# Kernel optimization log

Measured on AMD Instinct MI355X. Metric: run time of the kernel, lower is better.

Reference implementation:

```python
import jax, jax.numpy as jnp
import numpy as np

ANNEALING_SCALE = 0.1
BS, NV, S, D, V = 2, 16, 1024, 768, 50257

def setup_inputs() -> dict:
    key = jax.random.key(0)
    k1, k2, k3, k4, k5 = jax.random.split(key, 5)
    return {
        "input_ids": jax.random.randint(k1, (BS, S), 0, V),
        "content": jax.random.normal(k2, (BS, NV, S, D), dtype=jnp.float32),
        "contextualization": jax.random.normal(k3, (BS, NV, S, S), dtype=jnp.float32) * 0.05,
        "lm_head_weight": jax.random.normal(k4, (V, D), dtype=jnp.float32) * 0.02,
        "content_weights": jax.random.uniform(k5, (V, NV), dtype=jnp.float32),
    }

def reference(input_ids, content, contextualization, lm_head_weight, content_weights):
    bs, nv, s, d = content.shape
    # --- mask_annealing ---
    # Original computes relu(content @ W.T) over full vocab then gathers at input_ids.
    # Equivalent: gather rows of W first, then contract (same math since relu is
    # elementwise and only gathered columns are summed).
    Wg = lm_head_weight[input_ids]                              # (bs, s, d)
    sims = jnp.einsum('bkid,bjd->bkij', content, Wg)            # (bs, 16, s, s)
    sims = jnp.sum(jax.nn.relu(sims), axis=3)                   # (bs, 16, s)
    scores = jax.nn.sigmoid(-ANNEALING_SCALE * sims + 6.0)
    # upweight_nearby modifier
    scores = scores * (1.0 + jnp.arange(s, dtype=content.dtype) / 100.0)[None, None, :]
    scores = jnp.transpose(scores, (0, 2, 1))                   # (bs, s, 16)
    # --- create_content_soft_mask ---
    cw = content_weights[input_ids]                             # (bs, s, 16)
    weights = cw * scores + (1.0 - scores)                      # (bs, s, 16)
    # --- weighted sense combination ---
    content_m = content * jnp.transpose(weights, (0, 2, 1))[..., None]  # (bs,16,s,d)
    hidden = jnp.einsum('bkij,bkjd->bid', contextualization, content_m) # (bs, s, d)
    logits = hidden @ lm_head_weight.T                          # (bs, s, vocab)
    return logits
```

## Files before the change

kernel.cpp:

```cpp
#include <hip/hip_runtime.h>
#include <cstdint>
#include <cstddef>

#define BSZ 2
#define NV 16
#define SEQ 1024
#define DIM 768
#define VOC 50257
#define VOCP 50304

typedef unsigned int u32;
typedef unsigned short u16;
typedef _Float16 half8 __attribute__((ext_vector_type(8)));
typedef float f32x4 __attribute__((ext_vector_type(4)));

__device__ __forceinline__ u16 f2h(float f) {
  return __builtin_bit_cast(unsigned short, (_Float16)f);
}
__device__ __forceinline__ u32 pk2h(float a, float b) {
  return (u32)f2h(a) | ((u32)f2h(b) << 16);
}

__device__ __forceinline__ void gload16(const u16* g, u16* l) {
  __builtin_amdgcn_global_load_lds(
      (const __attribute__((address_space(1))) void*)g,
      (__attribute__((address_space(3))) void*)l, 16, 0, 0);
}

__global__ void k_prep_content(const float* __restrict__ content,
                               u16* __restrict__ cbf, u16* __restrict__ cT) {
  __shared__ u16 tile[32][33];
  const int bk = blockIdx.z;
  const int d0 = blockIdx.x * 32, j0 = blockIdx.y * 32;
  const float* src = content + (size_t)bk * SEQ * DIM;
  u16* dst = cbf + (size_t)bk * SEQ * DIM;
  u16* dstT = cT + (size_t)bk * DIM * SEQ;
  const int c = threadIdx.x;
#pragma unroll
  for (int rr = 0; rr < 4; ++rr) {
    const int r = threadIdx.y * 4 + rr;
    const float v = src[(size_t)(j0 + r) * DIM + d0 + c];
    const u16 bv = f2h(v);
    dst[(size_t)(j0 + r) * DIM + d0 + c] = bv;
    tile[r][c] = bv;
  }
  __syncthreads();
#pragma unroll
  for (int rr = 0; rr < 4; ++rr) {
    const int r = threadIdx.y * 4 + rr;
    dstT[(size_t)(d0 + r) * SEQ + j0 + c] = tile[c][r];
  }
}

__global__ void k_prep_w(const float* __restrict__ W, u16* __restrict__ Wb) {
  const int v = blockIdx.x;
  const int c = threadIdx.x * 4;
  u32 lo, hi;
  if (v < VOC) {
    const float4 f = *(const float4*)(W + (size_t)v * DIM + c);
    lo = pk2h(f.x, f.y); hi = pk2h(f.z, f.w);
  } else {
    lo = 0u; hi = 0u;
  }
  *(uint2*)(Wb + (size_t)v * DIM + c) = make_uint2(lo, hi);
}

__global__ void k_gather(const int* __restrict__ ids, const u16* __restrict__ Wb,
                         u16* __restrict__ Wg) {
  const int b = blockIdx.y, j = blockIdx.x;
  const int row = ids[b * SEQ + j];
  const int c = threadIdx.x * 4;
  *(uint2*)(Wg + ((size_t)b * SEQ + j) * DIM + c) =
      *(const uint2*)(Wb + (size_t)row * DIM + c);
}

__global__ void k_zero(float* __restrict__ p, int n) {
  const int i = blockIdx.x * 256 + threadIdx.x;
  if (i < n) p[i] = 0.f;
}

template <int LDA, int LDB>
__device__ __forceinline__ void gemm_core(const u16* __restrict__ A,
                                          const u16* __restrict__ B, int ksteps,
                                          u16* As, u16* Bs, f32x4 (&acc)[4][4],
                                          int t) {
  const int lane = t & 63, w = t >> 6, wr = w >> 1, wc = w & 1;
  const int rl = lane & 15;
  const int gsw = (((lane >> 4) ^ ((rl >> 1) & 3)) * 8);
  const int srow = 16 * w + (lane >> 2);
  const int sg = (((lane & 3) ^ ((lane >> 3) & 3)) * 8);
  const size_t gaBase = (size_t)srow * LDA + sg;
  const size_t gbBase = (size_t)srow * LDB + sg;
  u16* lA = As + w * 512;
  u16* lB = Bs + w * 512;

#define STAGE_(bb, kt)                                                  \
  {                                                                     \
    const u16* ga_ = A + gaBase + (size_t)(kt) * 32;                    \
    const u16* gb_ = B + gbBase + (size_t)(kt) * 32;                    \
    gload16(ga_, lA + (bb) * 4096);                                     \
    gload16(ga_ + (size_t)64 * LDA, lA + (bb) * 4096 + 2048);           \
    gload16(gb_, lB + (bb) * 4096);                                     \
    gload16(gb_ + (size_t)64 * LDB, lB + (bb) * 4096 + 2048);           \
  }

#define FRAGS_(bb)                                                      \
  half8 af[4], bf[4];                                                   \
  _Pragma("unroll") for (int m = 0; m < 4; ++m)                         \
      af[m] = *(const half8*)(As + (bb) * 4096 +                        \
                              (wr * 64 + m * 16 + rl) * 32 + gsw);      \
  _Pragma("unroll") for (int n = 0; n < 4; ++n)                         \
      bf[n] = *(const half8*)(Bs + (bb) * 4096 +                        \
                              (wc * 64 + n * 16 + rl) * 32 + gsw);      \
  _Pragma("unroll") for (int m = 0; m < 4; ++m)                         \
      _Pragma("unroll") for (int n = 0; n < 4; ++n)                     \
          acc[m][n] = __builtin_amdgcn_mfma_f32_16x16x32_f16(           \
              af[m], bf[n], acc[m][n], 0, 0, 0);

  STAGE_(0, 0);
  __syncthreads();
  int cur = 0;
  for (int kt = 0; kt < ksteps - 1; ++kt) {
    STAGE_(cur ^ 1, kt + 1);
    { FRAGS_(cur); }
    __syncthreads();
    cur ^= 1;
  }
  { FRAGS_(cur); }
#undef STAGE_
#undef FRAGS_
}

template <int LDA, int LDB>
__device__ __forceinline__ void gemm_ring2(const u16* __restrict__ A0,
                                           const u16* __restrict__ A1,
                                           const u16* __restrict__ B, int ksteps,
                                           u16* As0, u16* As1, u16* Bs,
                                           f32x4 (&acc0)[4][4],
                                           f32x4 (&acc1)[4][4], int t) {
  const int lane = t & 63, w = t >> 6, wr = w >> 1, wc = w & 1;
  const int rl = lane & 15;
  const int gsw = (((lane >> 4) ^ ((rl >> 1) & 3)) * 8);
  const int srow = 16 * w + (lane >> 2);
  const int sg = (((lane & 3) ^ ((lane >> 3) & 3)) * 8);
  const size_t gaBase = (size_t)srow * LDA + sg;
  const size_t gbBase = (size_t)srow * LDB + sg;
  const int wof = w * 512;

#define STG3_(ss, kt)                                                   \
  {                                                                     \
    const u16* ga0_ = A0 + gaBase + (size_t)(kt) * 32;                  \
    const u16* ga1_ = A1 + gaBase + (size_t)(kt) * 32;                  \
    const u16* gb_ = B + gbBase + (size_t)(kt) * 32;                    \
    gload16(ga0_, As0 + (ss) * 4096 + wof);                             \
    gload16(ga0_ + (size_t)64 * LDA, As0 + (ss) * 4096 + wof + 2048);   \
    gload16(ga1_, As1 + (ss) * 4096 + wof);                            \
    gload16(ga1_ + (size_t)64 * LDA, As1 + (ss) * 4096 + wof + 2048);   \
    gload16(gb_, Bs + (ss) * 4096 + wof);                              \
    gload16(gb_ + (size_t)64 * LDB, Bs + (ss) * 4096 + wof + 2048);     \
  }

#define FRAGS3_(ss)                                                     \
  half8 af0[4], af1[4], bf[4];                                          \
  _Pragma("unroll") for (int n = 0; n < 4; ++n)                         \
      bf[n] = *(const half8*)(Bs + (ss) * 4096 +                        \
                              (wc * 64 + n * 16 + rl) * 32 + gsw);      \
  _Pragma("unroll") for (int m = 0; m < 4; ++m)                         \
      af0[m] = *(const half8*)(As0 + (ss) * 4096 +                      \
                               (wr * 64 + m * 16 + rl) * 32 + gsw);     \
  _Pragma("unroll") for (int m = 0; m < 4; ++m)                         \
      af1[m] = *(const half8*)(As1 + (ss) * 4096 +                      \
                               (wr * 64 + m * 16 + rl) * 32 + gsw);

#define MFMA32_                                                         \
  __builtin_amdgcn_s_setprio(1);                                        \
  _Pragma("unroll") for (int m = 0; m < 4; ++m)                         \
      _Pragma("unroll") for (int n = 0; n < 4; ++n)                     \
          acc0[m][n] = __builtin_amdgcn_mfma_f32_16x16x32_f16(          \
              af0[m], bf[n], acc0[m][n], 0, 0, 0);                      \
  _Pragma("unroll") for (int m = 0; m < 4; ++m)                         \
      _Pragma("unroll") for (int n = 0; n < 4; ++n)                     \
          acc1[m][n] = __builtin_amdgcn_mfma_f32_16x16x32_f16(          \
              af1[m], bf[n], acc1[m][n], 0, 0, 0);                      \
  __builtin_amdgcn_s_setprio(0);

#define STEPF_(ss, kt)                                                  \
  asm volatile("s_waitcnt vmcnt(6)" ::: "memory");                      \
  __builtin_amdgcn_s_barrier();                                         \
  __builtin_amdgcn_sched_barrier(0);                                    \
  STG3_(((ss) + 2) % 3, (kt) + 2);                                      \
  { FRAGS3_(ss) MFMA32_ }

#define STEPL6_(ss)                                                     \
  asm volatile("s_waitcnt vmcnt(6)" ::: "memory");                      \
  __builtin_amdgcn_s_barrier();                                         \
  __builtin_amdgcn_sched_barrier(0);                                    \
  { FRAGS3_(ss) MFMA32_ }

#define STEPL0_(ss)                                                     \
  asm volatile("s_waitcnt vmcnt(0)" ::: "memory");                      \
  __builtin_amdgcn_s_barrier();                                         \
  __builtin_amdgcn_sched_barrier(0);                                    \
  { FRAGS3_(ss) MFMA32_ }

  STG3_(0, 0);
  STG3_(1, 1);
  const int nTrip = ksteps / 3;
  for (int u = 0; u < nTrip - 1; ++u) {
    const int kt = 3 * u;
    STEPF_(0, kt);
    STEPF_(1, kt + 1);
    STEPF_(2, kt + 2);
  }
  STEPF_(0, ksteps - 3);
  STEPL6_(1);
  STEPL0_(2);
#undef STG3_
#undef FRAGS3_
#undef MFMA32_
#undef STEPF_
#undef STEPL6_
#undef STEPL0_
}

__global__ __launch_bounds__(256, 2) void k_sims(const u16* __restrict__ cbf,
                                                 const u16* __restrict__ Wg,
                                                 float* __restrict__ sims) {
  __shared__ __align__(16) u16 As0[3 * 4096];
  __shared__ __align__(16) u16 As1[3 * 4096];
  __shared__ __align__(16) u16 Bs[3 * 4096];
  const int bk = blockIdx.z, b = bk >> 4;
  const int t = threadIdx.x;
  const int i0 = blockIdx.y * 256;
  const u16* A0 = cbf + (size_t)bk * SEQ * DIM + (size_t)i0 * DIM;
  const u16* A1 = A0 + (size_t)128 * DIM;
  const u16* B = Wg + (size_t)b * SEQ * DIM + (size_t)(blockIdx.x * 128) * DIM;
  f32x4 acc0[4][4] = {}, acc1[4][4] = {};
  gemm_ring2<DIM, DIM>(A0, A1, B, DIM / 32, As0, As1, Bs, acc0, acc1, t);
  const int lane = t & 63, w = t >> 6, wr = w >> 1;
  const int rg = lane >> 4, cl = lane & 15;
#pragma unroll
  for (int m = 0; m < 4; ++m) {
#pragma unroll
    for (int r = 0; r < 4; ++r) {
      float s0 = 0.f, s1 = 0.f;
#pragma unroll
      for (int n = 0; n < 4; ++n) {
        s0 += fmaxf(acc0[m][n][r], 0.f);
        s1 += fmaxf(acc1[m][n][r], 0.f);
      }
      s0 += __shfl_xor(s0, 1); s1 += __shfl_xor(s1, 1);
      s0 += __shfl_xor(s0, 2); s1 += __shfl_xor(s1, 2);
      s0 += __shfl_xor(s0, 4); s1 += __shfl_xor(s1, 4);
      s0 += __shfl_xor(s0, 8); s1 += __shfl_xor(s1, 8);
      if (cl == 0) {
        const int i = i0 + wr * 64 + m * 16 + rg * 4 + r;
        atomicAdd(&sims[(size_t)bk * SEQ + i], s0);
        atomicAdd(&sims[(size_t)bk * SEQ + i + 128], s1);
      }
    }
  }
}

__global__ void k_weights(const float* __restrict__ sims, const int* __restrict__ ids,
                          const float* __restrict__ cw, float* __restrict__ wtsT) {
  const int j = blockIdx.x * 256 + threadIdx.x;
  const int bk = blockIdx.y;
  const int b = bk >> 4, k = bk & 15;
  const float sm = sims[(size_t)bk * SEQ + j];
  float score = 1.f / (1.f + __expf(0.1f * sm - 6.f));
  score *= 1.f + (float)j * 0.01f;
  const int id = ids[b * SEQ + j];
  const float c = cw[(size_t)id * NV + k];
  wtsT[(size_t)bk * SEQ + j] = c * score + (1.f - score);
}

__global__ void k_ctx(const float* __restrict__ ctx, const float* __restrict__ wtsT,
                      u16* __restrict__ ctxw) {
  const size_t i = ((size_t)blockIdx.x * 256 + threadIdx.x) * 4;
  const float4 c = *(const float4*)(ctx + i);
  const size_t bk = i >> 20;
  const int j = (int)(i & (SEQ - 1));
  const float4 wv = *(const float4*)(wtsT + bk * SEQ + j);
  *(uint2*)(ctxw + i) =
      make_uint2(pk2h(c.x * wv.x, c.y * wv.y), pk2h(c.z * wv.z, c.w * wv.w));
}

__global__ __launch_bounds__(256) void k_hidden(const u16* __restrict__ ctxw,
                                                const u16* __restrict__ cT,
                                                float* __restrict__ part) {
  __shared__ __align__(16) u16 As[2 * 128 * 32];
  __shared__ __align__(16) u16 Bs[2 * 128 * 32];
  const int z = blockIdx.z;
  const int b = z >> 2, g = z & 3;
  const int i0 = blockIdx.y * 128, d0 = blockIdx.x * 128;
  const int t = threadIdx.x;
  f32x4 acc[4][4] = {};
  for (int kk = 0; kk < 4; ++kk) {
    const int sense = g * 4 + kk;
    const u16* A = ctxw + ((size_t)(b * NV + sense) * SEQ + i0) * SEQ;
    const u16* B = cT + ((size_t)(b * NV + sense) * DIM + d0) * SEQ;
    gemm_core<SEQ, SEQ>(A, B, SEQ / 32, As, Bs, acc, t);
    __syncthreads();
  }
  const int lane = t & 63, w = t >> 6, wr = w >> 1, wc = w & 1;
  const int rg = lane >> 4, cl = lane & 15;
  float* P = part + ((size_t)(g * BSZ + b) * SEQ + i0) * DIM + d0;
#pragma unroll
  for (int m = 0; m < 4; ++m)
#pragma unroll
    for (int n = 0; n < 4; ++n)
#pragma unroll
      for (int r = 0; r < 4; ++r)
        P[(size_t)(wr * 64 + m * 16 + rg * 4 + r) * DIM + wc * 64 + n * 16 + cl] =
            acc[m][n][r];
}

__global__ void k_reduce(const float* __restrict__ part, u16* __restrict__ hid) {
  const size_t i = ((size_t)blockIdx.x * 256 + threadIdx.x) * 4;
  const size_t NHID = (size_t)BSZ * SEQ * DIM;
  float4 s = {0.f, 0.f, 0.f, 0.f};
#pragma unroll
  for (int g = 0; g < 4; ++g) {
    const float4 p = *(const float4*)(part + (size_t)g * NHID + i);
    s.x += p.x; s.y += p.y; s.z += p.z; s.w += p.w;
  }
  *(uint2*)(hid + i) = make_uint2(pk2h(s.x, s.y), pk2h(s.z, s.w));
}

__global__ __launch_bounds__(256, 2) void k_logits(const u16* __restrict__ hid,
                                                   const u16* __restrict__ Wb,
                                                   float* __restrict__ out) {
  __shared__ __align__(16) u16 As0[3 * 4096];
  __shared__ __align__(16) u16 As1[3 * 4096];
  __shared__ __align__(16) u16 Bs[3 * 4096];
  const int bid = blockIdx.x;
  const int swz = (bid & 7) * 393 + (bid >> 3);
  const int it = swz & 7, vt = swz >> 3;
  const int i0 = it * 256, v0 = vt * 128;
  const int t = threadIdx.x;
  const u16* A0 = hid + (size_t)i0 * DIM;
  const u16* A1 = A0 + (size_t)128 * DIM;
  const u16* B = Wb + (size_t)v0 * DIM;
  f32x4 acc0[4][4] = {}, acc1[4][4] = {};
  gemm_ring2<DIM, DIM>(A0, A1, B, DIM / 32, As0, As1, Bs, acc0, acc1, t);
  const int lane = t & 63, w = t >> 6, wr = w >> 1, wc = w & 1;
  const int rg = lane >> 4, cl = lane & 15;
#pragma unroll
  for (int m = 0; m < 4; ++m)
#pragma unroll
    for (int n = 0; n < 4; ++n) {
      const int vv = v0 + wc * 64 + n * 16 + cl;
      if (vv < VOC) {
        const int i = i0 + wr * 64 + m * 16 + rg * 4;
#pragma unroll
        for (int r = 0; r < 4; ++r)
          out[(size_t)(i + r) * VOC + vv] = acc0[m][n][r];
#pragma unroll
        for (int r = 0; r < 4; ++r)
          out[(size_t)(i + 128 + r) * VOC + vv] = acc1[m][n][r];
      }
    }
}

extern "C" void kernel_launch(void* const* d_in, const int* in_sizes, int n_in,
                              void* d_out, int out_size, void* d_ws, size_t ws_size,
                              hipStream_t stream) {
  const int* ids = (const int*)d_in[0];
  const float* content = (const float*)d_in[1];
  const float* ctx = (const float*)d_in[2];
  const float* W = (const float*)d_in[3];
  const float* cw = (const float*)d_in[4];
  float* out = (float*)d_out;
  char* ws = (char*)d_ws;

  u16* cbf  = (u16*)(ws);
  u16* cT   = (u16*)(ws + 50331648);
  u16* Wb   = (u16*)(ws + 100663296);
  u16* Wg   = (u16*)(ws + 177930240);
  u16* ctxw = (u16*)(ws + 181075968);
  float* sims = (float*)(ws + 248184832);
  float* wtsT = (float*)(ws + 248315904);
  float* part = (float*)cbf;
  u16* hid = Wg;

  k_prep_content<<<dim3(DIM / 32, SEQ / 32, BSZ * NV), dim3(32, 8), 0, stream>>>(
      content, cbf, cT);
  k_prep_w<<<VOCP, 192, 0, stream>>>(W, Wb);
  k_gather<<<dim3(SEQ, BSZ), 192, 0, stream>>>(ids, Wb, Wg);
  k_zero<<<128, 256, 0, stream>>>(sims, BSZ * NV * SEQ);
  k_sims<<<dim3(8, 4, BSZ * NV), 256, 0, stream>>>(cbf, Wg, sims);
  k_weights<<<dim3(4, BSZ * NV), 256, 0, stream>>>(sims, ids, cw, wtsT);
  k_ctx<<<32768, 256, 0, stream>>>(ctx, wtsT, ctxw);
  k_hidden<<<dim3(6, 8, 8), 256, 0, stream>>>(ctxw, cT, part);
  k_reduce<<<1536, 256, 0, stream>>>(part, hid);
  k_logits<<<8 * 393, 256, 0, stream>>>(hid, Wb, out);
}
```

Before: 591.4 us.

## Rewrite logits GEMM with 256x256 tiles, 8 waves and 8-slot LDS ring

```diff
diff --git a/kernel.cpp b/kernel.cpp
--- a/kernel.cpp
+++ b/kernel.cpp
@@ -328,37 +328,100 @@
   *(uint2*)(hid + i) = make_uint2(pk2h(s.x, s.y), pk2h(s.z, s.w));
 }
 
-__global__ __launch_bounds__(256, 2) void k_logits(const u16* __restrict__ hid,
+__global__ __launch_bounds__(512, 2) void k_logits(const u16* __restrict__ hid,
                                                    const u16* __restrict__ Wb,
                                                    float* __restrict__ out) {
-  __shared__ __align__(16) u16 As0[3 * 4096];
-  __shared__ __align__(16) u16 As1[3 * 4096];
-  __shared__ __align__(16) u16 Bs[3 * 4096];
+  __shared__ __align__(16) u16 lds[8 * 8192];
   const int bid = blockIdx.x;
-  const int swz = (bid & 7) * 393 + (bid >> 3);
+  const int swz = (bid & 7) * 197 + (bid >> 3);
   const int it = swz & 7, vt = swz >> 3;
-  const int i0 = it * 256, v0 = vt * 128;
+  const int i0 = it * 256;
+  const int v0 = (vt == 196) ? (VOCP - 256) : vt * 256;
   const int t = threadIdx.x;
-  const u16* A0 = hid + (size_t)i0 * DIM;
-  const u16* A1 = A0 + (size_t)128 * DIM;
-  const u16* B = Wb + (size_t)v0 * DIM;
-  f32x4 acc0[4][4] = {}, acc1[4][4] = {};
-  gemm_ring2<DIM, DIM>(A0, A1, B, DIM / 32, As0, As1, Bs, acc0, acc1, t);
-  const int lane = t & 63, w = t >> 6, wr = w >> 1, wc = w & 1;
-  const int rg = lane >> 4, cl = lane & 15;
-#pragma unroll
-  for (int m = 0; m < 4; ++m)
+  const int lane = t & 63, w = t >> 6;
+  const int wm = w >> 2, wn = w & 3;
+  const int rl = lane & 15, kg = lane >> 4;
+  const int gsw = (kg ^ ((rl >> 1) & 3)) * 8;
+  const int gi = w * 64 + lane;
+  const int srow = gi >> 2;
+  const int sgr = ((gi & 3) ^ ((srow >> 1) & 3)) * 8;
+  const u16* Abase = hid + (size_t)i0 * DIM;
+  const u16* Bbase = Wb + (size_t)v0 * DIM;
+  u16* ldst = lds + w * 512 + lane * 8;
+
+#define STG(slot, base, koff)                                         \
+  {                                                                   \
+    const u16* s_ = (base) + (size_t)srow * DIM + (koff) + sgr;       \
+    gload16(s_, ldst + (slot) * 8192);                                \
+    gload16(s_ + (size_t)128 * DIM, ldst + (slot) * 8192 + 4096);     \
+  }
+
+#define COMPUTE(sA, sB)                                               \
+  {                                                                   \
+    half8 bf[4], af[8];                                               \
+    _Pragma("unroll") for (int n = 0; n < 4; ++n)                     \
+        bf[n] = *(const half8*)(lds + (sB) * 8192 +                   \
+                                (wn * 64 + n * 16 + rl) * 32 + gsw);  \
+    _Pragma("unroll") for (int m = 0; m < 8; ++m)                     \
+        af[m] = *(const half8*)(lds + (sA) * 8192 +                   \
+                                (wm * 128 + m * 16 + rl) * 32 + gsw); \
+    __builtin_amdgcn_s_setprio(1);                                    \
+    _Pragma("unroll") for (int m = 0; m < 8; ++m)                     \
+        _Pragma("unroll") for (int n = 0; n < 4; ++n)                 \
+            acc[m][n] = __builtin_amdgcn_mfma_f32_16x16x32_f16(       \
+                af[m], bf[n], acc[m][n], 0, 0, 0);                    \
+    __builtin_amdgcn_s_setprio(0);                                    \
+  }
+
+#define WAITB(N)                                          \
+  asm volatile("s_waitcnt vmcnt(" #N ")" ::: "memory");   \
+  __builtin_amdgcn_s_barrier();                           \
+  __builtin_amdgcn_sched_barrier(0);
+
+  f32x4 acc[8][4] = {};
+  STG(0, Abase, 0);
+  STG(1, Bbase, 0);
+  STG(2, Abase, 32);
+  STG(3, Bbase, 32);
+  STG(4, Abase, 64);
+  STG(5, Bbase, 64);
+
+  for (int tau = 0; tau < 10; ++tau) {
+    const int tp = (tau & 1) * 4;
+    const int kb = tau * 64;
+    WAITB(8);
+    STG((tp + 6) & 7, Abase, kb + 96);
+    STG((tp + 7) & 7, Bbase, kb + 96);
+    COMPUTE(tp, tp + 1);
+    WAITB(8);
+    STG((tp + 8) & 7, Abase, kb + 128);
+    STG((tp + 9) & 7, Bbase, kb + 128);
+    COMPUTE(tp + 2, tp + 3);
+  }
+  WAITB(8);
+  STG(6, Abase, 736);
+  STG(7, Bbase, 736);
+  COMPUTE(0, 1);
+  WAITB(8);
+  COMPUTE(2, 3);
+  WAITB(4);
+  COMPUTE(4, 5);
+  WAITB(0);
+  COMPUTE(6, 7);
+#undef STG
+#undef COMPUTE
+#undef WAITB
+
+#pragma unroll
+  for (int m = 0; m < 8; ++m)
 #pragma unroll
     for (int n = 0; n < 4; ++n) {
-      const int vv = v0 + wc * 64 + n * 16 + cl;
+      const int vv = v0 + wn * 64 + n * 16 + rl;
       if (vv < VOC) {
-        const int i = i0 + wr * 64 + m * 16 + rg * 4;
+        const int ib = i0 + wm * 128 + m * 16 + kg * 4;
 #pragma unroll
         for (int r = 0; r < 4; ++r)
-          out[(size_t)(i + r) * VOC + vv] = acc0[m][n][r];
-#pragma unroll
-        for (int r = 0; r < 4; ++r)
-          out[(size_t)(i + 128 + r) * VOC + vv] = acc1[m][n][r];
+          out[(size_t)(ib + r) * VOC + vv] = acc[m][n][r];
       }
     }
 }
@@ -394,5 +457,5 @@
   k_ctx<<<32768, 256, 0, stream>>>(ctx, wtsT, ctxw);
   k_hidden<<<dim3(6, 8, 8), 256, 0, stream>>>(ctxw, cT, part);
   k_reduce<<<1536, 256, 0, stream>>>(part, hid);
-  k_logits<<<8 * 393, 256, 0, stream>>>(hid, Wb, out);
-}
+  k_logits<<<8 * 197, 512, 0, stream>>>(hid, Wb, out);
+}
```

New measurement: 587.1 us. No clear change (-0.7%).
